# Optimization experiments

Measured on AMD Instinct MI355X. Metric: run time of the kernel, lower is better.

The kernel has to match this reference:

```python
import jax, jax.numpy as jnp
import numpy as np

N_NODES = 50000
N_EDGES = 300000
D_IN = 256
D_HID = 256


def setup_inputs() -> dict:
    key = jax.random.key(0)
    ks = jax.random.split(key, 9)
    x = jax.random.normal(ks[0], (N_NODES, D_IN), dtype=jnp.float32)
    src = jax.random.randint(ks[1], (N_EDGES,), 0, N_NODES, dtype=jnp.int64)
    dst = jax.random.randint(ks[2], (N_EDGES,), 0, N_NODES, dtype=jnp.int64)
    # Kaiming-uniform-ish init like nn.Linear defaults
    def lin(k, fan_in, fan_out):
        bound = 1.0 / np.sqrt(fan_in)
        kw, kb = jax.random.split(k)
        W = jax.random.uniform(kw, (fan_out, fan_in), minval=-bound, maxval=bound, dtype=jnp.float32)
        b = jax.random.uniform(kb, (fan_out,), minval=-bound, maxval=bound, dtype=jnp.float32)
        return W, b
    W1, b1 = lin(ks[3], 2 * D_IN, D_HID)
    W2, b2 = lin(ks[4], D_HID, D_HID)
    W3, b3 = lin(ks[5], D_HID, 1)
    return {"x": x, "src": src, "dst": dst,
            "W1": W1, "b1": b1, "W2": W2, "b2": b2, "W3": W3, "b3": b3}


def reference(x, src, dst, W1, b1, W2, b2, W3, b3):
    # gather src/dst node features per edge and concat -> [E, 2*D_IN]
    h = jnp.concatenate([x[src], x[dst]], axis=1)
    h = jax.nn.relu(h @ W1.T + b1)          # [E, D_HID]
    h = jax.nn.relu(h @ W2.T + b2)          # dropout is identity in eval mode
    score = h @ W3.T + b3                   # [E, 1]
    return score
```

## Files before the change

kernel.cpp:

```cpp
#include <hip/hip_runtime.h>

typedef short bfx8 __attribute__((ext_vector_type(8)));
typedef float fx4 __attribute__((ext_vector_type(4)));

#define D 256
#define E_TILE 64

__device__ __forceinline__ float b2f(short s) {
  union { unsigned u; float f; } v; v.u = ((unsigned)(unsigned short)s) << 16; return v.f;
}
__device__ __forceinline__ short f2b(float f) {
  union { float f; unsigned u; } v; v.f = f;
  unsigned u = v.u;
  u += 0x7fffu + ((u >> 16) & 1u);
  return (short)(u >> 16);
}
__device__ __forceinline__ float relu(float f) { return f > 0.f ? f : 0.f; }

__global__ void k_prep(const float* __restrict__ W1, const float* __restrict__ W2,
                       unsigned short* __restrict__ B1, unsigned short* __restrict__ W2b) {
  int t = blockIdx.x * 256 + threadIdx.x;
  if (t < 512 * 256) {
    int n = t >> 8, k = t & 255;
    float v = (n < 256) ? W1[n * 512 + k] : W1[(n - 256) * 512 + 256 + k];
    B1[t] = (unsigned short)f2b(v);
  } else if (t < 512 * 256 + 256 * 256) {
    int i = t - 512 * 256;
    W2b[i] = (unsigned short)f2b(W2[i]);
  }
}

__launch_bounds__(512, 1)
__global__ void k_node(const float* __restrict__ x, const unsigned short* __restrict__ B1,
                       const float* __restrict__ b1,
                       unsigned short* __restrict__ PQ, int n_nodes, int ntiles) {
  __shared__ __align__(16) short smA[64 * 264];
  short* smT = smA;
  const int tid = threadIdx.x;
  const int wave = tid >> 6, lane = tid & 63;
  const int lr = lane & 15, lg = lane >> 4;

  bfx8 bw[4][8];
  float b1v[4];
#pragma unroll
  for (int nt = 0; nt < 4; ++nt) {
    int n = wave * 64 + nt * 16 + lr;
    b1v[nt] = (n < 256) ? b1[n] : 0.f;
#pragma unroll
    for (int ks = 0; ks < 8; ++ks)
      bw[nt][ks] = *(const bfx8*)(B1 + n * 256 + ks * 32 + lg * 8);
  }

  const int r  = tid >> 3;
  const int c4 = (tid & 7) * 4;
  const int rs = tid >> 4;
  const int cs = (tid & 15) * 8;

  for (int tile = blockIdx.x; tile < ntiles; tile += gridDim.x) {
    const int m0 = tile * 64;
    {
      int m = m0 + r;
      if (m < n_nodes) {
        const float* p = x + (size_t)m * 256 + c4;
#pragma unroll
        for (int j = 0; j < 8; ++j) {
          float4 v = *(const float4*)(p + j * 32);
          short4 o = { f2b(v.x), f2b(v.y), f2b(v.z), f2b(v.w) };
          *(short4*)&smA[r * 264 + c4 + j * 32] = o;
        }
      } else {
        short4 z = {0, 0, 0, 0};
#pragma unroll
        for (int j = 0; j < 8; ++j)
          *(short4*)&smA[r * 264 + c4 + j * 32] = z;
      }
    }
    __syncthreads();

    fx4 acc[4][4] = {};
#pragma unroll
    for (int ks = 0; ks < 8; ++ks) {
      bfx8 af[4];
#pragma unroll
      for (int mt = 0; mt < 4; ++mt)
        af[mt] = *(const bfx8*)&smA[(mt * 16 + lr) * 264 + ks * 32 + lg * 8];
#pragma unroll
      for (int nt = 0; nt < 4; ++nt)
#pragma unroll
        for (int mt = 0; mt < 4; ++mt)
          acc[mt][nt] = __builtin_amdgcn_mfma_f32_16x16x32_bf16(af[mt], bw[nt][ks], acc[mt][nt], 0, 0, 0);
    }
    __syncthreads();

#pragma unroll
    for (int h = 0; h < 2; ++h) {
#pragma unroll
      for (int mt2 = 0; mt2 < 2; ++mt2) {
        const int mt = 2 * h + mt2;
#pragma unroll
        for (int nt = 0; nt < 4; ++nt)
#pragma unroll
          for (int i = 0; i < 4; ++i) {
            int mrow = mt2 * 16 + lg * 4 + i;
            int n = wave * 64 + nt * 16 + lr;
            smT[mrow * 520 + n] = f2b(acc[mt][nt][i] + b1v[nt]);
          }
      }
      __syncthreads();
      int m = m0 + h * 32 + rs;
      if (m < n_nodes) {
#pragma unroll
        for (int j = 0; j < 4; ++j) {
          int c = cs + j * 128;
          *(bfx8*)(PQ + (size_t)m * 512 + c) = *(const bfx8*)&smT[rs * 520 + c];
        }
      }
      __syncthreads();
    }
  }
}

__launch_bounds__(256, 2)
__global__ void k_edge(const unsigned short* __restrict__ PQ,
                       const int* __restrict__ src, const int* __restrict__ dst,
                       const unsigned short* __restrict__ W2b,
                       const float* __restrict__ b2, const float* __restrict__ W3,
                       const float* __restrict__ b3, float* __restrict__ out,
                       int E, int ntiles) {
  __shared__ __align__(16) short smH[64 * 264];
  __shared__ float smS[4][64];
  const int tid = threadIdx.x;
  const int wave = tid >> 6, lane = tid & 63;
  const int lr = lane & 15, lg = lane >> 4;

  bfx8 bw[4][8];
  float b2v[4], w3v[4];
#pragma unroll
  for (int nt = 0; nt < 4; ++nt) {
    int n = wave * 64 + nt * 16 + lr;
    b2v[nt] = b2[n];
    w3v[nt] = W3[n];
#pragma unroll
    for (int ks = 0; ks < 8; ++ks)
      bw[nt][ks] = *(const bfx8*)(W2b + n * 256 + ks * 32 + lg * 8);
  }
  const float b3v = b3[0];

  for (int tile = blockIdx.x; tile < ntiles; tile += gridDim.x) {
    const int base = tile * E_TILE;
    {
      int r = tid >> 2;
      int e = base + r;
      if (e < E) {
        int s = src[e], d = dst[e];
        const unsigned short* ps = PQ + (size_t)s * 512;
        const unsigned short* pd = PQ + (size_t)d * 512 + 256;
#pragma unroll
        for (int it = 0; it < 8; ++it) {
          int c = (tid & 3) * 8 + it * 32;
          bfx8 pv = *(const bfx8*)(ps + c);
          bfx8 qv = *(const bfx8*)(pd + c);
          bfx8 o;
#pragma unroll
          for (int j = 0; j < 8; ++j)
            o[j] = f2b(relu(b2f(pv[j]) + b2f(qv[j])));
          *(bfx8*)&smH[r * 264 + c] = o;
        }
      } else {
        bfx8 z = (bfx8){0,0,0,0,0,0,0,0};
#pragma unroll
        for (int it = 0; it < 8; ++it) {
          int c = (tid & 3) * 8 + it * 32;
          *(bfx8*)&smH[r * 264 + c] = z;
        }
      }
    }
    __syncthreads();

    fx4 acc[4][4] = {};
#pragma unroll
    for (int ks = 0; ks < 8; ++ks) {
      bfx8 af[4];
#pragma unroll
      for (int mt = 0; mt < 4; ++mt)
        af[mt] = *(const bfx8*)&smH[(mt * 16 + lr) * 264 + ks * 32 + lg * 8];
#pragma unroll
      for (int nt = 0; nt < 4; ++nt)
#pragma unroll
        for (int mt = 0; mt < 4; ++mt)
          acc[mt][nt] = __builtin_amdgcn_mfma_f32_16x16x32_bf16(af[mt], bw[nt][ks], acc[mt][nt], 0, 0, 0);
    }

#pragma unroll
    for (int mt = 0; mt < 4; ++mt)
#pragma unroll
      for (int i = 0; i < 4; ++i) {
        float p = 0.f;
#pragma unroll
        for (int nt = 0; nt < 4; ++nt)
          p += relu(acc[mt][nt][i] + b2v[nt]) * w3v[nt];
        p += __shfl_xor(p, 1);
        p += __shfl_xor(p, 2);
        p += __shfl_xor(p, 4);
        p += __shfl_xor(p, 8);
        if (lr == 0) smS[wave][mt * 16 + lg * 4 + i] = p;
      }
    __syncthreads();
    if (tid < 64) {
      int e = base + tid;
      if (e < E) out[e] = smS[0][tid] + smS[1][tid] + smS[2][tid] + smS[3][tid] + b3v;
    }
  }
}

__global__ void k_fallback(const float* __restrict__ x, const int* __restrict__ src,
                           const int* __restrict__ dst, const float* __restrict__ W1,
                           const float* __restrict__ b1, const float* __restrict__ W2,
                           const float* __restrict__ b2, const float* __restrict__ W3,
                           const float* __restrict__ b3, float* __restrict__ out, int E) {
  __shared__ float smF[4][512];
  __shared__ float smG[4][256];
  int wave = threadIdx.x >> 6, lane = threadIdx.x & 63;
  int e = blockIdx.x * 4 + wave;
  bool valid = e < E;
  int ec = valid ? e : 0;
  int s = src[ec], d = dst[ec];
  for (int j = 0; j < 8; ++j) {
    int k = lane * 8 + j;
    smF[wave][k] = (k < 256) ? x[(size_t)s * 256 + k] : x[(size_t)d * 256 + k - 256];
  }
  __syncthreads();
  for (int t = 0; t < 4; ++t) {
    int n = lane + t * 64;
    float a = b1[n];
    for (int k = 0; k < 512; ++k) a += smF[wave][k] * W1[n * 512 + k];
    smG[wave][n] = relu(a);
  }
  __syncthreads();
  float p = 0.f;
  for (int t = 0; t < 4; ++t) {
    int n = lane + t * 64;
    float a = b2[n];
    for (int k = 0; k < 256; ++k) a += smG[wave][k] * W2[n * 256 + k];
    p += relu(a) * W3[n];
  }
  for (int m = 1; m < 64; m <<= 1) p += __shfl_xor(p, m);
  if (lane == 0 && valid) out[e] = p + b3[0];
}

extern "C" void kernel_launch(void* const* d_in, const int* in_sizes, int n_in,
                              void* d_out, int out_size, void* d_ws, size_t ws_size,
                              hipStream_t stream) {
  const float* x  = (const float*)d_in[0];
  const int*   src = (const int*)d_in[1];
  const int*   dst = (const int*)d_in[2];
  const float* W1 = (const float*)d_in[3];
  const float* b1 = (const float*)d_in[4];
  const float* W2 = (const float*)d_in[5];
  const float* b2 = (const float*)d_in[6];
  const float* W3 = (const float*)d_in[7];
  const float* b3 = (const float*)d_in[8];
  float* out = (float*)d_out;

  const int E = in_sizes[1];
  const int n_nodes = in_sizes[0] / 256;

  const size_t offB1 = 0;
  const size_t offW2 = (size_t)512 * 256 * 2;
  const size_t offPQ = offW2 + (size_t)256 * 256 * 2;
  const size_t need = offPQ + (size_t)n_nodes * 512 * 2;

  if (ws_size >= need) {
    unsigned short* B1  = (unsigned short*)((char*)d_ws + offB1);
    unsigned short* W2b = (unsigned short*)((char*)d_ws + offW2);
    unsigned short* PQ  = (unsigned short*)((char*)d_ws + offPQ);
    k_prep<<<768, 256, 0, stream>>>(W1, W2, B1, W2b);
    const int ntiles_node = (n_nodes + 63) / 64;
    k_node<<<256, 512, 0, stream>>>(x, B1, b1, PQ, n_nodes, ntiles_node);
    const int ntiles = (E + E_TILE - 1) / E_TILE;
    k_edge<<<512, 256, 0, stream>>>(PQ, src, dst, W2b, b2, W3, b3, out, E, ntiles);
  } else {
    k_fallback<<<(E + 3) / 4, 256, 0, stream>>>(x, src, dst, W1, b1, W2, b2, W3, b3, out, E);
  }
}
```

Before: 209.5 us.

## Prefetch next edge tile's gathered node rows into LDS with async direct loads

Replaces the per-thread register gather of source and destination node rows with `global_load_lds` direct-to-LDS loads into a new raw staging buffer. The loads for the next tile are issued before the current tile's MFMA work, so gather latency can overlap with compute. The grid is halved to 256 blocks, one tile stream per CU, because the larger LDS footprint removes the second resident block. The risk is lower occupancy, and correctness depends on the load-to-LDS completing before the barrier.

```diff
diff --git a/kernel.cpp b/kernel.cpp
--- a/kernel.cpp
+++ b/kernel.cpp
@@ -120,6 +120,26 @@
   }
 }
 
+__device__ __forceinline__ void stage_tile(const unsigned short* __restrict__ PQ,
+                                           const int* __restrict__ src,
+                                           const int* __restrict__ dst,
+                                           short* smRaw, int ebase, int w, int lane, int E) {
+  int eidx = ebase + w * 16 + (lane & 15);
+  if (eidx > E - 1) eidx = E - 1;
+  int vs = src[eidx];
+  int vd = dst[eidx];
+  const char* pqc = (const char*)PQ;
+#pragma unroll
+  for (int i = 0; i < 16; ++i) {
+    int ss = __builtin_amdgcn_readlane(vs, i);
+    int sd = __builtin_amdgcn_readlane(vd, i);
+    const char* gp = (lane < 32)
+        ? pqc + (size_t)ss * 1024 + (size_t)lane * 16
+        : pqc + (size_t)sd * 1024 + 512 + (size_t)(lane - 32) * 16;
+    __builtin_amdgcn_global_load_lds((const void*)gp, (void*)&smRaw[(w * 16 + i) * 520], 16, 0, 0);
+  }
+}
+
 __launch_bounds__(256, 2)
 __global__ void k_edge(const unsigned short* __restrict__ PQ,
                        const int* __restrict__ src, const int* __restrict__ dst,
@@ -127,11 +147,13 @@
                        const float* __restrict__ b2, const float* __restrict__ W3,
                        const float* __restrict__ b3, float* __restrict__ out,
                        int E, int ntiles) {
+  __shared__ __align__(16) short smRaw[64 * 520];
   __shared__ __align__(16) short smH[64 * 264];
   __shared__ float smS[4][64];
   const int tid = threadIdx.x;
   const int wave = tid >> 6, lane = tid & 63;
   const int lr = lane & 15, lg = lane >> 4;
+  const int G = gridDim.x;
 
   bfx8 bw[4][8];
   float b2v[4], w3v[4];
@@ -146,36 +168,28 @@
   }
   const float b3v = b3[0];
 
-  for (int tile = blockIdx.x; tile < ntiles; tile += gridDim.x) {
-    const int base = tile * E_TILE;
-    {
-      int r = tid >> 2;
-      int e = base + r;
-      if (e < E) {
-        int s = src[e], d = dst[e];
-        const unsigned short* ps = PQ + (size_t)s * 512;
-        const unsigned short* pd = PQ + (size_t)d * 512 + 256;
-#pragma unroll
-        for (int it = 0; it < 8; ++it) {
-          int c = (tid & 3) * 8 + it * 32;
-          bfx8 pv = *(const bfx8*)(ps + c);
-          bfx8 qv = *(const bfx8*)(pd + c);
-          bfx8 o;
-#pragma unroll
-          for (int j = 0; j < 8; ++j)
-            o[j] = f2b(relu(b2f(pv[j]) + b2f(qv[j])));
-          *(bfx8*)&smH[r * 264 + c] = o;
-        }
-      } else {
-        bfx8 z = (bfx8){0,0,0,0,0,0,0,0};
-#pragma unroll
-        for (int it = 0; it < 8; ++it) {
-          int c = (tid & 3) * 8 + it * 32;
-          *(bfx8*)&smH[r * 264 + c] = z;
-        }
-      }
-    }
-    __syncthreads();
+  const int r = tid >> 2, cb = (tid & 3) * 8;
+  const int t0 = blockIdx.x;
+
+  if (t0 < ntiles) stage_tile(PQ, src, dst, smRaw, t0 * E_TILE, wave, lane, E);
+  __syncthreads();
+
+  for (int t = t0; t < ntiles; t += G) {
+#pragma unroll
+    for (int it = 0; it < 8; ++it) {
+      int c = cb + it * 32;
+      bfx8 pv = *(const bfx8*)&smRaw[r * 520 + c];
+      bfx8 qv = *(const bfx8*)&smRaw[r * 520 + 256 + c];
+      bfx8 o;
+#pragma unroll
+      for (int j = 0; j < 8; ++j)
+        o[j] = f2b(relu(b2f(pv[j]) + b2f(qv[j])));
+      *(bfx8*)&smH[r * 264 + c] = o;
+    }
+    __syncthreads();
+
+    if (t + G < ntiles)
+      stage_tile(PQ, src, dst, smRaw, (t + G) * E_TILE, wave, lane, E);
 
     fx4 acc[4][4] = {};
 #pragma unroll
@@ -207,7 +221,7 @@
       }
     __syncthreads();
     if (tid < 64) {
-      int e = base + tid;
+      int e = t * E_TILE + tid;
       if (e < E) out[e] = smS[0][tid] + smS[1][tid] + smS[2][tid] + smS[3][tid] + b3v;
     }
   }
@@ -278,7 +292,7 @@
     const int ntiles_node = (n_nodes + 63) / 64;
     k_node<<<256, 512, 0, stream>>>(x, B1, b1, PQ, n_nodes, ntiles_node);
     const int ntiles = (E + E_TILE - 1) / E_TILE;
-    k_edge<<<512, 256, 0, stream>>>(PQ, src, dst, W2b, b2, W3, b3, out, E, ntiles);
+    k_edge<<<256, 256, 0, stream>>>(PQ, src, dst, W2b, b2, W3, b3, out, E, ntiles);
   } else {
     k_fallback<<<(E + 3) / 4, 256, 0, stream>>>(x, src, dst, W1, b1, W2, b2, W3, b3, out, E);
   }
```

Measured after the change: 260.3 us. 1.24x slower.
